# Kernel optimization log

Hardware: AMD Instinct MI355X
Metric: run time of the kernel (lower is better)

## Reference

```python
import jax, jax.numpy as jnp
import numpy as np

N_NODES = 100000
N_EDGES = 3200000
D_IN = 256
D_OUT = 256


def setup_inputs() -> dict:
    key = jax.random.key(0)
    k1, k2, k3, k4, k5, k6 = jax.random.split(key, 6)
    x = jax.random.normal(k1, (N_NODES, D_IN), dtype=jnp.float32)
    edge_src = jax.random.randint(k2, (N_EDGES,), 0, N_NODES, dtype=jnp.int32)
    edge_dst = jax.random.randint(k3, (N_EDGES,), 0, N_NODES, dtype=jnp.int32)
    edge_weight = jax.random.uniform(k4, (N_EDGES,), dtype=jnp.float32)
    weight = jax.random.normal(k5, (D_IN, D_OUT), dtype=jnp.float32) * 0.02
    bias = jax.random.uniform(k6, (D_OUT,), dtype=jnp.float32)
    return {"x": x, "edge_src": edge_src, "edge_dst": edge_dst,
            "edge_weight": edge_weight, "weight": weight, "bias": bias}


def reference(x, edge_src, edge_dst, edge_weight, weight, bias):
    # support = X @ W  (dense GEMM)
    support = x @ weight  # [N, D_OUT]
    # output = A @ support, A given as COO edges (dst <- src with weight)
    msgs = support[edge_src] * edge_weight[:, None]  # [E, D_OUT]
    out = jax.ops.segment_sum(msgs, edge_dst, num_segments=N_NODES)  # [N, D_OUT]
    return out + bias
```

## Files before the change

kernel.cpp:

```cpp
#include <hip/hip_runtime.h>
#include <hip/hip_bf16.h>

#define N_NODES 100000
#define N_EDGES 3200000
#define DDIM    256
#define M_PAD   100096
#define NBKT    782
#define BCAP    4608
#define EPB     4096
#define NB_BINA 782
#define NB_GEMM 1564
#define GCAP    2432
#define SMEM_BYTES 50432

typedef __attribute__((ext_vector_type(8))) short short8;
typedef __attribute__((ext_vector_type(4))) float f32x4;

typedef const __attribute__((address_space(1))) void gvoid_t;
typedef __attribute__((address_space(3))) void lvoid_t;

__device__ __forceinline__ void load_lds16(const void* g, void* l) {
  __builtin_amdgcn_global_load_lds((gvoid_t*)g, (lvoid_t*)l, 16, 0, 0);
}

__device__ __forceinline__ unsigned short f2bf(float f) {
  __hip_bfloat16 h = __float2bfloat16(f);
  return *(unsigned short*)&h;
}
__device__ __forceinline__ float bflo(unsigned u) { return __uint_as_float(u << 16); }
__device__ __forceinline__ float bfhi(unsigned u) { return __uint_as_float(u & 0xffff0000u); }

__global__ void convw_kernel(const float* __restrict__ w, unsigned short* __restrict__ wt,
                             int* __restrict__ gcur) {
  int t = blockIdx.x * blockDim.x + threadIdx.x;
  int n = t >> 8, k = t & 255;
  wt[t] = f2bf(w[k * 256 + n]);
  if (t < NBKT) gcur[t] = 0;
}

__global__ __launch_bounds__(256, 3) void gemm_binA_kernel(
    const float* __restrict__ x, const unsigned short* __restrict__ wt,
    unsigned short* __restrict__ sup,
    const int* __restrict__ src, const int* __restrict__ dst,
    const float* __restrict__ wgt,
    int* __restrict__ gcur, unsigned long long* __restrict__ region) {
  __shared__ __align__(16) char smem[SMEM_BYTES];
  const int bid = blockIdx.x;
  const int t = threadIdx.x;

  if (bid >= NB_BINA) {
    unsigned short* As0 = (unsigned short*)smem;
    unsigned short* Bs0 = (unsigned short*)(smem + 8192);
    unsigned short* As1 = (unsigned short*)(smem + 16384);
    unsigned short* Bs1 = (unsigned short*)(smem + 24576);
    const int g  = bid - NB_BINA;
    const int m0 = (g >> 1) * 128;
    const int n0 = (g & 1) * 128;
    const int w    = t >> 6;
    const int lane = t & 63;
    const int quad = lane >> 4;
    const int l15  = lane & 15;
    const int wr   = w >> 1, wc = w & 1;
    const int srow   = lane >> 2;
    const int schunk = (lane & 3) * 8;

    f32x4 acc[4][4] = {};

#define A_LOAD(kt, va)                                                        \
    do { _Pragma("unroll")                                                    \
      for (int j = 0; j < 4; ++j) {                                           \
        int row = j * 32 + (t >> 3);                                          \
        int xr = m0 + row; if (xr >= N_NODES) xr = N_NODES - 1;               \
        va[j] = *(const float4*)(x + (size_t)xr * 256 + (kt) + (t & 7) * 4);  \
      } } while (0)
#define A_STORE(va, asb)                                                      \
    do { _Pragma("unroll")                                                    \
      for (int j = 0; j < 4; ++j) {                                           \
        int row = j * 32 + (t >> 3);                                          \
        ushort4 o;                                                            \
        o.x = f2bf(va[j].x); o.y = f2bf(va[j].y);                             \
        o.z = f2bf(va[j].z); o.w = f2bf(va[j].w);                             \
        *(ushort4*)((asb) + row * 32 + (t & 7) * 4) = o;                      \
      } } while (0)
#define B_LOAD(kt, bsb)                                                       \
    do { _Pragma("unroll")                                                    \
      for (int i = 0; i < 2; ++i) {                                           \
        int r = w * 32 + i * 16 + srow;                                       \
        load_lds16(wt + ((size_t)(n0 + r) * 256 + (kt) + schunk),             \
                   (bsb) + (w * 32 + i * 16) * 32);                           \
      } } while (0)
#define COMPUTE(asb, bsb)                                                     \
    do {                                                                      \
      short8 a[4], b[4];                                                      \
      _Pragma("unroll")                                                       \
      for (int mi = 0; mi < 4; ++mi)                                          \
        a[mi] = *(const short8*)((asb) + (wr * 64 + mi * 16 + l15) * 32 + quad * 8); \
      _Pragma("unroll")                                                       \
      for (int ni = 0; ni < 4; ++ni)                                          \
        b[ni] = *(const short8*)((bsb) + (wc * 64 + ni * 16 + l15) * 32 + quad * 8); \
      _Pragma("unroll")                                                       \
      for (int mi = 0; mi < 4; ++mi)                                          \
        _Pragma("unroll")                                                     \
        for (int ni = 0; ni < 4; ++ni)                                        \
          acc[mi][ni] = __builtin_amdgcn_mfma_f32_16x16x32_bf16(a[mi], b[ni], acc[mi][ni], 0, 0, 0); \
    } while (0)

    {
      float4 va[4];
      A_LOAD(0, va);
      A_STORE(va, As0);
      B_LOAD(0, Bs0);
    }
    __syncthreads();
    for (int kp = 0; kp < 4; ++kp) {
      const int kt1 = kp * 64 + 32;
      {
        float4 va[4];
        A_LOAD(kt1, va);
        COMPUTE(As0, Bs0);
        A_STORE(va, As1);
        B_LOAD(kt1, Bs1);
      }
      __syncthreads();
      if (kp < 3) {
        const int kt2 = kp * 64 + 64;
        float4 vb[4];
        A_LOAD(kt2, vb);
        COMPUTE(As1, Bs1);
        A_STORE(vb, As0);
        B_LOAD(kt2, Bs0);
      } else {
        COMPUTE(As1, Bs1);
      }
      __syncthreads();
    }

#pragma unroll
    for (int mi = 0; mi < 4; ++mi) {
#pragma unroll
      for (int r = 0; r < 4; ++r) {
        size_t row = (size_t)(m0 + wr * 64 + mi * 16 + quad * 4 + r);
#pragma unroll
        for (int ni = 0; ni < 4; ++ni) {
          int col = n0 + wc * 64 + ni * 16 + l15;
          sup[row * 256 + col] = f2bf(acc[mi][ni][r]);
        }
      }
    }
    return;
  }

  unsigned long long* staged = (unsigned long long*)smem;
  unsigned short* sbkt = (unsigned short*)(smem + 32768);
  int* lstart = (int*)(smem + 40960);
  int* lcur   = (int*)(smem + 44088);
  int* gb     = (int*)(smem + 47216);
  int* lhist  = (int*)smem;
  int* csum   = (int*)(smem + 3200);

  const int e0 = bid * EPB;
  const int ecnt = min(EPB, N_EDGES - e0);

  for (int i = t; i < NBKT; i += 256) lhist[i] = 0;
  __syncthreads();
  for (int k = t; k < ecnt; k += 256)
    atomicAdd(&lhist[dst[e0 + k] >> 7], 1);
  __syncthreads();

  int i0 = 4 * t;
  int a0 = (i0 + 0 < NBKT) ? lhist[i0 + 0] : 0;
  int a1 = (i0 + 1 < NBKT) ? lhist[i0 + 1] : 0;
  int a2 = (i0 + 2 < NBKT) ? lhist[i0 + 2] : 0;
  int a3 = (i0 + 3 < NBKT) ? lhist[i0 + 3] : 0;
  int s = a0 + a1 + a2 + a3;
  csum[t] = s;
  __syncthreads();
  for (int off = 1; off < 256; off <<= 1) {
    int v = (t >= off) ? csum[t - off] : 0;
    __syncthreads();
    csum[t] += v;
    __syncthreads();
  }
  int base = csum[t] - s;
  if (i0 + 0 < NBKT) lstart[i0 + 0] = base; base += a0;
  if (i0 + 1 < NBKT) lstart[i0 + 1] = base; base += a1;
  if (i0 + 2 < NBKT) lstart[i0 + 2] = base; base += a2;
  if (i0 + 3 < NBKT) lstart[i0 + 3] = base;
  __syncthreads();

  for (int i = t; i < NBKT; i += 256) {
    int c = lhist[i];
    int off = c ? atomicAdd(&gcur[i], c) : 0;
    gb[i] = i * BCAP + off;
    lcur[i] = lstart[i];
  }
  __syncthreads();

  for (int k = t; k < ecnt; k += 256) {
    int d  = dst[e0 + k];
    int sr = src[e0 + k];
    float wv = wgt[e0 + k];
    int b = d >> 7;
    int p = atomicAdd(&lcur[b], 1);
    staged[p] = ((unsigned long long)__float_as_uint(wv) << 32) |
                ((unsigned)(d & 127) << 17) | (unsigned)sr;
    sbkt[p] = (unsigned short)b;
  }
  __syncthreads();

  for (int j = t; j < ecnt; j += 256) {
    int b = sbkt[j];
    int addr = gb[b] + (j - lstart[b]);
    if (addr < (b + 1) * BCAP) region[addr] = staged[j];
  }
}

__global__ __launch_bounds__(256) void csr_gather_kernel(
    const unsigned long long* __restrict__ region,
    const int* __restrict__ gcur,
    const unsigned short* __restrict__ sup,
    const float* __restrict__ bias,
    float* __restrict__ out) {
  __shared__ unsigned long long lcsr[GCAP];
  __shared__ int lhist[64], loff[64], lcur[64];
  const int t = threadIdx.x;
  const int b = blockIdx.x;
  const int h = blockIdx.y;
  const int cnt = min(gcur[b], BCAP);
  const int base = b * BCAP;

  if (t < 64) lhist[t] = 0;
  __syncthreads();
  for (int j = t; j < cnt; j += 256) {
    unsigned lo = (unsigned)(region[base + j] & 0xffffffffu);
    int dl = (int)((lo >> 17) & 127);
    if ((dl >> 6) == h) atomicAdd(&lhist[dl & 63], 1);
  }
  __syncthreads();
  if (t < 64) loff[t] = lhist[t];
  __syncthreads();
  for (int off = 1; off < 64; off <<= 1) {
    int v = (t >= off && t < 64) ? loff[t - off] : 0;
    __syncthreads();
    if (t < 64) loff[t] += v;
    __syncthreads();
  }
  if (t < 64) { loff[t] -= lhist[t]; lcur[t] = loff[t]; }
  __syncthreads();
  for (int j = t; j < cnt; j += 256) {
    unsigned long long e = region[base + j];
    int dl = (int)((e >> 17) & 127);
    if ((dl >> 6) == h) {
      int p = atomicAdd(&lcur[dl & 63], 1);
      if (p < GCAP) lcsr[p] = e;
    }
  }
  __syncthreads();

  const int wv = t >> 6;
  const int c0 = (t & 63) * 4;
  float4 bv = *(const float4*)(bias + c0);

  for (int dl = wv; dl < 64; dl += 4) {
    int node = b * 128 + h * 64 + dl;
    if (node >= N_NODES) continue;
    int start = loff[dl];
    int end   = min(lcur[dl], GCAP);
    float a0 = bv.x, a1 = bv.y, a2 = bv.z, a3 = bv.w;

    int i = start;
    for (; i + 2 <= end; i += 2) {
      unsigned long long m0 = lcsr[i];
      unsigned long long m1 = lcsr[i + 1];
      int   s0 = (int)(m0 & 0x1ffffu);
      float w0 = __uint_as_float((unsigned)(m0 >> 32));
      int   s1 = (int)(m1 & 0x1ffffu);
      float w1 = __uint_as_float((unsigned)(m1 >> 32));
      uint2 p0 = *(const uint2*)(sup + (size_t)s0 * 256 + c0);
      uint2 p1 = *(const uint2*)(sup + (size_t)s1 * 256 + c0);
      a0 = fmaf(w0, bflo(p0.x), a0);
      a1 = fmaf(w0, bfhi(p0.x), a1);
      a2 = fmaf(w0, bflo(p0.y), a2);
      a3 = fmaf(w0, bfhi(p0.y), a3);
      a0 = fmaf(w1, bflo(p1.x), a0);
      a1 = fmaf(w1, bfhi(p1.x), a1);
      a2 = fmaf(w1, bflo(p1.y), a2);
      a3 = fmaf(w1, bfhi(p1.y), a3);
    }
    if (i < end) {
      unsigned long long m0 = lcsr[i];
      int   s0 = (int)(m0 & 0x1ffffu);
      float w0 = __uint_as_float((unsigned)(m0 >> 32));
      uint2 p0 = *(const uint2*)(sup + (size_t)s0 * 256 + c0);
      a0 = fmaf(w0, bflo(p0.x), a0);
      a1 = fmaf(w0, bfhi(p0.x), a1);
      a2 = fmaf(w0, bflo(p0.y), a2);
      a3 = fmaf(w0, bfhi(p0.y), a3);
    }
    *(float4*)(out + (size_t)node * 256 + c0) = make_float4(a0, a1, a2, a3);
  }
}

extern "C" void kernel_launch(void* const* d_in, const int* in_sizes, int n_in,
                              void* d_out, int out_size, void* d_ws, size_t ws_size,
                              hipStream_t stream) {
  const float* x        = (const float*)d_in[0];
  const int*   edge_src = (const int*)d_in[1];
  const int*   edge_dst = (const int*)d_in[2];
  const float* edge_w   = (const float*)d_in[3];
  const float* weight   = (const float*)d_in[4];
  const float* bias     = (const float*)d_in[5];
  float* out = (float*)d_out;

  char* ws = (char*)d_ws;
  size_t off = 0;
  auto alloc = [&](size_t bytes) -> void* {
    void* p = ws + off;
    off = (off + bytes + 255) & ~(size_t)255;
    return p;
  };

  unsigned short* wt  = (unsigned short*)alloc(256 * 256 * 2);
  unsigned short* sup = (unsigned short*)alloc((size_t)M_PAD * 256 * 2);
  unsigned long long* region = (unsigned long long*)alloc((size_t)NBKT * BCAP * 8);
  int* gcur = (int*)alloc(NBKT * 4);

  convw_kernel<<<256, 256, 0, stream>>>(weight, wt, gcur);
  gemm_binA_kernel<<<NB_BINA + NB_GEMM, 256, 0, stream>>>(x, wt, sup,
                                                          edge_src, edge_dst, edge_w,
                                                          gcur, region);
  csr_gather_kernel<<<dim3(NBKT, 2), 256, 0, stream>>>(region, gcur, sup, bias, out);
}
```

Before: 495.1 us.

## Restructure GEMM LDS layout, register-staged B loads, and LDS-staged coalesced output

The GEMM part of the fused kernel now stores A and B tiles in LDS in a k-chunk-major layout with padded stride to avoid bank conflicts on the MFMA operand reads. The B tile is loaded through registers instead of direct global-to-LDS loads, and the pipeline becomes a single unrolled 8-step double-buffered loop. The output tile is staged through padded LDS and written with 16-byte coalesced stores instead of scattered 2-byte stores. This costs more register pressure and an extra LDS round trip plus a barrier at the epilogue.

```diff
diff --git a/kernel.cpp b/kernel.cpp
--- a/kernel.cpp
+++ b/kernel.cpp
@@ -13,15 +13,13 @@
 #define GCAP    2432
 #define SMEM_BYTES 50432
 
+#define QS 1040
+
 typedef __attribute__((ext_vector_type(8))) short short8;
 typedef __attribute__((ext_vector_type(4))) float f32x4;
 
 typedef const __attribute__((address_space(1))) void gvoid_t;
 typedef __attribute__((address_space(3))) void lvoid_t;
-
-__device__ __forceinline__ void load_lds16(const void* g, void* l) {
-  __builtin_amdgcn_global_load_lds((gvoid_t*)g, (lvoid_t*)l, 16, 0, 0);
-}
 
 __device__ __forceinline__ unsigned short f2bf(float f) {
   __hip_bfloat16 h = __float2bfloat16(f);
@@ -50,9 +48,9 @@
 
   if (bid >= NB_BINA) {
     unsigned short* As0 = (unsigned short*)smem;
-    unsigned short* Bs0 = (unsigned short*)(smem + 8192);
-    unsigned short* As1 = (unsigned short*)(smem + 16384);
-    unsigned short* Bs1 = (unsigned short*)(smem + 24576);
+    unsigned short* Bs0 = (unsigned short*)(smem + 8320);
+    unsigned short* As1 = (unsigned short*)(smem + 16640);
+    unsigned short* Bs1 = (unsigned short*)(smem + 24960);
     const int g  = bid - NB_BINA;
     const int m0 = (g >> 1) * 128;
     const int n0 = (g & 1) * 128;
@@ -61,43 +59,49 @@
     const int quad = lane >> 4;
     const int l15  = lane & 15;
     const int wr   = w >> 1, wc = w & 1;
-    const int srow   = lane >> 2;
-    const int schunk = (lane & 3) * 8;
 
     f32x4 acc[4][4] = {};
 
-#define A_LOAD(kt, va)                                                        \
+#define A_LOADG(kt, va)                                                       \
     do { _Pragma("unroll")                                                    \
       for (int j = 0; j < 4; ++j) {                                           \
         int row = j * 32 + (t >> 3);                                          \
         int xr = m0 + row; if (xr >= N_NODES) xr = N_NODES - 1;               \
         va[j] = *(const float4*)(x + (size_t)xr * 256 + (kt) + (t & 7) * 4);  \
       } } while (0)
-#define A_STORE(va, asb)                                                      \
+#define A_STOREL(va, asb)                                                     \
     do { _Pragma("unroll")                                                    \
       for (int j = 0; j < 4; ++j) {                                           \
         int row = j * 32 + (t >> 3);                                          \
+        int c = t & 7;                                                        \
         ushort4 o;                                                            \
         o.x = f2bf(va[j].x); o.y = f2bf(va[j].y);                             \
         o.z = f2bf(va[j].z); o.w = f2bf(va[j].w);                             \
-        *(ushort4*)((asb) + row * 32 + (t & 7) * 4) = o;                      \
+        *(ushort4*)((asb) + (c >> 1) * QS + row * 8 + (c & 1) * 4) = o;       \
       } } while (0)
-#define B_LOAD(kt, bsb)                                                       \
+#define B_LOADG(kt, vb)                                                       \
     do { _Pragma("unroll")                                                    \
-      for (int i = 0; i < 2; ++i) {                                           \
-        int r = w * 32 + i * 16 + srow;                                       \
-        load_lds16(wt + ((size_t)(n0 + r) * 256 + (kt) + schunk),             \
-                   (bsb) + (w * 32 + i * 16) * 32);                           \
+      for (int j = 0; j < 2; ++j) {                                           \
+        int f = j * 256 + t;                                                  \
+        int row = f >> 2, c2 = f & 3;                                         \
+        vb[j] = *(const short8*)(wt + (size_t)(n0 + row) * 256 + (kt) + c2 * 8); \
+      } } while (0)
+#define B_STOREL(vb, bsb)                                                     \
+    do { _Pragma("unroll")                                                    \
+      for (int j = 0; j < 2; ++j) {                                           \
+        int f = j * 256 + t;                                                  \
+        int row = f >> 2, c2 = f & 3;                                         \
+        *(short8*)((bsb) + c2 * QS + row * 8) = vb[j];                        \
       } } while (0)
 #define COMPUTE(asb, bsb)                                                     \
     do {                                                                      \
       short8 a[4], b[4];                                                      \
       _Pragma("unroll")                                                       \
       for (int mi = 0; mi < 4; ++mi)                                          \
-        a[mi] = *(const short8*)((asb) + (wr * 64 + mi * 16 + l15) * 32 + quad * 8); \
+        a[mi] = *(const short8*)((asb) + quad * QS + (wr * 64 + mi * 16 + l15) * 8); \
       _Pragma("unroll")                                                       \
       for (int ni = 0; ni < 4; ++ni)                                          \
-        b[ni] = *(const short8*)((bsb) + (wc * 64 + ni * 16 + l15) * 32 + quad * 8); \
+        b[ni] = *(const short8*)((bsb) + quad * QS + (wc * 64 + ni * 16 + l15) * 8); \
       _Pragma("unroll")                                                       \
       for (int mi = 0; mi < 4; ++mi)                                          \
         _Pragma("unroll")                                                     \
@@ -106,46 +110,40 @@
     } while (0)
 
     {
-      float4 va[4];
-      A_LOAD(0, va);
-      A_STORE(va, As0);
-      B_LOAD(0, Bs0);
-    }
-    __syncthreads();
-    for (int kp = 0; kp < 4; ++kp) {
-      const int kt1 = kp * 64 + 32;
-      {
-        float4 va[4];
-        A_LOAD(kt1, va);
-        COMPUTE(As0, Bs0);
-        A_STORE(va, As1);
-        B_LOAD(kt1, Bs1);
-      }
+      float4 va[4]; short8 vb[2];
+      A_LOADG(0, va); B_LOADG(0, vb);
+      A_STOREL(va, As0); B_STOREL(vb, Bs0);
+    }
+    __syncthreads();
+#pragma unroll
+    for (int kp = 0; kp < 8; ++kp) {
+      unsigned short* Ac = (kp & 1) ? As1 : As0;
+      unsigned short* Bc = (kp & 1) ? Bs1 : Bs0;
+      unsigned short* An = (kp & 1) ? As0 : As1;
+      unsigned short* Bn = (kp & 1) ? Bs0 : Bs1;
+      float4 va[4]; short8 vb[2];
+      if (kp < 7) { A_LOADG((kp + 1) * 32, va); B_LOADG((kp + 1) * 32, vb); }
+      COMPUTE(Ac, Bc);
+      if (kp < 7) { A_STOREL(va, An); B_STOREL(vb, Bn); }
       __syncthreads();
-      if (kp < 3) {
-        const int kt2 = kp * 64 + 64;
-        float4 vb[4];
-        A_LOAD(kt2, vb);
-        COMPUTE(As1, Bs1);
-        A_STORE(vb, As0);
-        B_LOAD(kt2, Bs0);
-      } else {
-        COMPUTE(As1, Bs1);
-      }
-      __syncthreads();
-    }
-
-#pragma unroll
-    for (int mi = 0; mi < 4; ++mi) {
-#pragma unroll
-      for (int r = 0; r < 4; ++r) {
-        size_t row = (size_t)(m0 + wr * 64 + mi * 16 + quad * 4 + r);
-#pragma unroll
-        for (int ni = 0; ni < 4; ++ni) {
-          int col = n0 + wc * 64 + ni * 16 + l15;
-          sup[row * 256 + col] = f2bf(acc[mi][ni][r]);
-        }
-      }
+    }
+
+    unsigned short* Cs = (unsigned short*)smem;
+#pragma unroll
+    for (int mi = 0; mi < 4; ++mi)
+#pragma unroll
+      for (int ni = 0; ni < 4; ++ni)
+#pragma unroll
+        for (int r = 0; r < 4; ++r)
+          Cs[(wr * 64 + mi * 16 + quad * 4 + r) * 136 + wc * 64 + ni * 16 + l15] =
+              f2bf(acc[mi][ni][r]);
+    __syncthreads();
+#pragma unroll
+    for (int i = 0; i < 8; ++i) {
+      int ch = i * 256 + t;
+      int r = ch >> 4, cc = (ch & 15) * 8;
+      short8 v = *(const short8*)(Cs + r * 136 + cc);
+      *(short8*)(sup + (size_t)(m0 + r) * 256 + n0 + cc) = v;
     }
     return;
   }
```

New measurement: 492.4 us. Within noise of the previous version (-0.5%).
